# Kernel optimization log

Measured on AMD Instinct MI355X. Metric: run time of the kernel, lower is better.

## Reference

```python
import jax, jax.numpy as jnp
import numpy as np

B, D, K, L = 16384, 255, 4, 16  # batch, destinations, tunnels/dst, outgoing links
T = D * K                        # total tunnels = 1020
EPS = 1e-8


def setup_inputs() -> dict:
    key = jax.random.key(0)
    k1, k2, k3, k4, k5 = jax.random.split(key, 5)
    pred_ratios = jax.random.uniform(k1, (B, T), dtype=jnp.float32)
    demands = jax.random.uniform(k2, (B, D), dtype=jnp.float32) * 100.0
    current_link_utils = jax.random.uniform(k3, (B, L), dtype=jnp.float32)
    link_capacities = jax.random.uniform(k4, (L,), dtype=jnp.float32) * 900.0 + 100.0
    tunnel_to_link = jax.random.randint(k5, (T,), 0, L, dtype=jnp.int32)
    return {
        "pred_ratios": pred_ratios,
        "demands": demands,
        "current_link_utils": current_link_utils,
        "link_capacities": link_capacities,
        "tunnel_to_link": tunnel_to_link,
    }


def reference(pred_ratios, demands, current_link_utils, link_capacities, tunnel_to_link):
    # Equal group sizes: destination d owns tunnels [d*K, (d+1)*K)
    Tn = pred_ratios.shape[1]
    Dn = demands.shape[1]
    Kn = Tn // Dn
    Ln = link_capacities.shape[0]
    # tunnel_traffic[b, t] = demand[b, dst(t)] * ratio[b, t]
    tunnel_traffic = pred_ratios * jnp.repeat(demands, Kn, axis=1)  # [B, T]
    # scatter-add tunnels into links, expressed as a dense [T, L] one-hot GEMM
    onehot = jax.nn.one_hot(tunnel_to_link, Ln, dtype=pred_ratios.dtype)  # [T, L]
    node_link_traffic = tunnel_traffic @ onehot  # [B, L]
    node_link_util = node_link_traffic / (link_capacities[None, :] + EPS)
    variance_loss = jnp.var(node_link_util, axis=1, ddof=1).mean()  # torch.var is unbiased
    congestion_penalty = (node_link_util * current_link_utils).sum(axis=1).mean()
    max_util_loss = node_link_util.max(axis=1).mean()
    return 0.3 * variance_loss + 0.5 * congestion_penalty + 0.2 * max_util_loss
```

## Files before the change

kernel.cpp:

```cpp
#include <hip/hip_runtime.h>

constexpr int T_TUN = 1020;
constexpr int D_DST = 255;
constexpr int L_LNK = 16;
constexpr float EPS = 1e-8f;
constexpr int ROWS_PER_BLOCK = 8;
constexpr int ROWS_PER_WAVE  = 2;
constexpr int PSTRIDE = 16;

__global__ __launch_bounds__(256) void rowloss_kernel(
    const float* __restrict__ pred,
    const float* __restrict__ demands,
    const float* __restrict__ cur,
    const float* __restrict__ caps,
    const int*   __restrict__ t2l,
    float* __restrict__ partials)
{
  const int tid  = threadIdx.x;
  const int lane = tid & 63;
  const int w    = tid >> 6;

  __shared__ float priv_all[4][64 * PSTRIDE];
  __shared__ float wacc[4];
  float* priv = priv_all[w];
  float* mine = priv + lane * PSTRIDE;

  const int b16 = lane & 15;
  const float capinv = 1.0f / (caps[b16] + EPS);

  int off[4][4];
  bool dv[4];
#pragma unroll
  for (int j = 0; j < 4; ++j) {
    const int d = lane + 64 * j;
    dv[j] = (d < D_DST);
    const int dd = dv[j] ? d : 0;
    const int4 lk = ((const int4*)t2l)[dd];
    off[j][0] = lane * PSTRIDE + lk.x;
    off[j][1] = lane * PSTRIDE + lk.y;
    off[j][2] = lane * PSTRIDE + lk.z;
    off[j][3] = lane * PSTRIDE + lk.w;
  }

  float acc = 0.0f;
  const int row0 = blockIdx.x * ROWS_PER_BLOCK + w * ROWS_PER_WAVE;

#pragma unroll
  for (int r = 0; r < ROWS_PER_WAVE; ++r) {
    const int b = row0 + r;

    __builtin_amdgcn_wave_barrier();

    const float4 z = make_float4(0.f, 0.f, 0.f, 0.f);
    float4* mz = (float4*)mine;
    mz[0] = z; mz[1] = z; mz[2] = z; mz[3] = z;

    const float  mycur = cur[(size_t)b * L_LNK + b16];
    const float4* prow = (const float4*)(pred + (size_t)b * T_TUN);
    const float*  drow = demands + (size_t)b * D_DST;

#pragma unroll
    for (int j = 0; j < 4; ++j) {
      if (!dv[j]) continue;
      const int d = lane + 64 * j;
      const float4 r4 = prow[d];
      const float dem = drow[d];
      priv[off[j][0]] += r4.x * dem;
      priv[off[j][1]] += r4.y * dem;
      priv[off[j][2]] += r4.z * dem;
      priv[off[j][3]] += r4.w * dem;
    }

    __builtin_amdgcn_wave_barrier();

    float cs = 0.0f;
#pragma unroll
    for (int k = 0; k < 16; ++k) cs += priv[lane + 64 * k];
    cs += __shfl_xor(cs, 16, 64);
    cs += __shfl_xor(cs, 32, 64);

    const float u = cs * capinv;
    float s1 = u, s2 = u * u, s3 = u * mycur, mx = u;
#pragma unroll
    for (int m = 1; m < 16; m <<= 1) {
      s1 += __shfl_xor(s1, m, 64);
      s2 += __shfl_xor(s2, m, 64);
      s3 += __shfl_xor(s3, m, 64);
      const float o = __shfl_xor(mx, m, 64);
      mx = fmaxf(mx, o);
    }
    const float mean = s1 * (1.0f / 16.0f);
    const float var  = (s2 - 16.0f * mean * mean) * (1.0f / 15.0f);
    acc += 0.3f * var + 0.5f * s3 + 0.2f * mx;
  }

  if (lane == 0) wacc[w] = acc;
  __syncthreads();
  if (tid == 0) partials[blockIdx.x] = wacc[0] + wacc[1] + wacc[2] + wacc[3];
}

__global__ __launch_bounds__(256) void reduce_kernel(
    const float* __restrict__ partials, int n, float* __restrict__ out, float invB)
{
  __shared__ float s[256];
  const int tid = threadIdx.x;
  float a = 0.0f;
  for (int i = tid; i < n; i += 256) a += partials[i];
  s[tid] = a;
  __syncthreads();
  for (int st = 128; st > 0; st >>= 1) {
    if (tid < st) s[tid] += s[tid + st];
    __syncthreads();
  }
  if (tid == 0) out[0] = s[0] * invB;
}

extern "C" void kernel_launch(void* const* d_in, const int* in_sizes, int n_in,
                              void* d_out, int out_size, void* d_ws, size_t ws_size,
                              hipStream_t stream) {
  const float* pred    = (const float*)d_in[0];
  const float* demands = (const float*)d_in[1];
  const float* cur     = (const float*)d_in[2];
  const float* caps    = (const float*)d_in[3];
  const int*   t2l     = (const int*)d_in[4];
  float* out = (float*)d_out;

  const int L = in_sizes[3];
  const int B = in_sizes[2] / L;

  const int grid = B / ROWS_PER_BLOCK;
  float* partials = (float*)d_ws;

  rowloss_kernel<<<grid, 256, 0, stream>>>(pred, demands, cur, caps, t2l, partials);
  reduce_kernel<<<1, 256, 0, stream>>>(partials, grid, out, 1.0f / (float)B);
}
```

Baseline: 111.3 us.

## Transpose LDS histogram layout, use LDS atomics, merge reductions, drop reduce kernel

Reorganizes the per-wave shared histogram from lane-major with stride 16 to link-major with stride 64, and accumulates with LDS float atomics, which changes the bank-conflict pattern of the scatter. The column reads use a rotated index to avoid conflicts. The four butterfly reductions (sum, sum of squares, weighted sum, max) become one shuffle chain, with each 16-lane group handling one statistic, followed by readlanes. The final reduce kernel is replaced by a global atomicAdd per block plus a tiny zeroing kernel, which makes the summation order nondeterministic.

```diff
diff --git a/kernel.cpp b/kernel.cpp
--- a/kernel.cpp
+++ b/kernel.cpp
@@ -6,7 +6,11 @@
 constexpr float EPS = 1e-8f;
 constexpr int ROWS_PER_BLOCK = 8;
 constexpr int ROWS_PER_WAVE  = 2;
-constexpr int PSTRIDE = 16;
+
+__device__ __forceinline__ float read_lane_f(float v, int l) {
+  return __builtin_bit_cast(float,
+      __builtin_amdgcn_readlane(__builtin_bit_cast(int, v), l));
+}
 
 __global__ __launch_bounds__(256) void rowloss_kernel(
     const float* __restrict__ pred,
@@ -14,18 +18,18 @@
     const float* __restrict__ cur,
     const float* __restrict__ caps,
     const int*   __restrict__ t2l,
-    float* __restrict__ partials)
+    float* __restrict__ out, float invB)
 {
   const int tid  = threadIdx.x;
   const int lane = tid & 63;
   const int w    = tid >> 6;
 
-  __shared__ float priv_all[4][64 * PSTRIDE];
+  __shared__ float priv_all[4][L_LNK * 64];
   __shared__ float wacc[4];
   float* priv = priv_all[w];
-  float* mine = priv + lane * PSTRIDE;
 
   const int b16 = lane & 15;
+  const int g   = lane >> 4;
   const float capinv = 1.0f / (caps[b16] + EPS);
 
   int off[4][4];
@@ -36,11 +40,13 @@
     dv[j] = (d < D_DST);
     const int dd = dv[j] ? d : 0;
     const int4 lk = ((const int4*)t2l)[dd];
-    off[j][0] = lane * PSTRIDE + lk.x;
-    off[j][1] = lane * PSTRIDE + lk.y;
-    off[j][2] = lane * PSTRIDE + lk.z;
-    off[j][3] = lane * PSTRIDE + lk.w;
+    off[j][0] = lk.x * 64 + lane;
+    off[j][1] = lk.y * 64 + lane;
+    off[j][2] = lk.z * 64 + lane;
+    off[j][3] = lk.w * 64 + lane;
   }
+
+  const int rbase = b16 * 64 + g * 16;
 
   float acc = 0.0f;
   const int row0 = blockIdx.x * ROWS_PER_BLOCK + w * ROWS_PER_WAVE;
@@ -51,9 +57,12 @@
 
     __builtin_amdgcn_wave_barrier();
 
-    const float4 z = make_float4(0.f, 0.f, 0.f, 0.f);
-    float4* mz = (float4*)mine;
-    mz[0] = z; mz[1] = z; mz[2] = z; mz[3] = z;
+    {
+      const float4 z = make_float4(0.f, 0.f, 0.f, 0.f);
+      float4* pz = (float4*)priv;
+#pragma unroll
+      for (int i = 0; i < 4; ++i) pz[lane + 64 * i] = z;
+    }
 
     const float  mycur = cur[(size_t)b * L_LNK + b16];
     const float4* prow = (const float4*)(pred + (size_t)b * T_TUN);
@@ -65,55 +74,45 @@
       const int d = lane + 64 * j;
       const float4 r4 = prow[d];
       const float dem = drow[d];
-      priv[off[j][0]] += r4.x * dem;
-      priv[off[j][1]] += r4.y * dem;
-      priv[off[j][2]] += r4.z * dem;
-      priv[off[j][3]] += r4.w * dem;
+      unsafeAtomicAdd(&priv[off[j][0]], r4.x * dem);
+      unsafeAtomicAdd(&priv[off[j][1]], r4.y * dem);
+      unsafeAtomicAdd(&priv[off[j][2]], r4.z * dem);
+      unsafeAtomicAdd(&priv[off[j][3]], r4.w * dem);
     }
 
     __builtin_amdgcn_wave_barrier();
 
     float cs = 0.0f;
 #pragma unroll
-    for (int k = 0; k < 16; ++k) cs += priv[lane + 64 * k];
+    for (int k = 0; k < 16; ++k) cs += priv[rbase + ((k + b16) & 15)];
     cs += __shfl_xor(cs, 16, 64);
     cs += __shfl_xor(cs, 32, 64);
 
     const float u = cs * capinv;
-    float s1 = u, s2 = u * u, s3 = u * mycur, mx = u;
+
+    float val = (g == 0) ? u : (g == 1) ? (u * u) : (g == 2) ? (u * mycur) : u;
 #pragma unroll
     for (int m = 1; m < 16; m <<= 1) {
-      s1 += __shfl_xor(s1, m, 64);
-      s2 += __shfl_xor(s2, m, 64);
-      s3 += __shfl_xor(s3, m, 64);
-      const float o = __shfl_xor(mx, m, 64);
-      mx = fmaxf(mx, o);
+      const float o  = __shfl_xor(val, m, 64);
+      const float sm = val + o;
+      const float mm = fmaxf(val, o);
+      val = (g == 3) ? mm : sm;
     }
-    const float mean = s1 * (1.0f / 16.0f);
-    const float var  = (s2 - 16.0f * mean * mean) * (1.0f / 15.0f);
+    const float s1 = read_lane_f(val, 0);
+    const float s2 = read_lane_f(val, 16);
+    const float s3 = read_lane_f(val, 32);
+    const float mx = read_lane_f(val, 48);
+
+    const float var = (s2 - s1 * s1 * (1.0f / 16.0f)) * (1.0f / 15.0f);
     acc += 0.3f * var + 0.5f * s3 + 0.2f * mx;
   }
 
   if (lane == 0) wacc[w] = acc;
   __syncthreads();
-  if (tid == 0) partials[blockIdx.x] = wacc[0] + wacc[1] + wacc[2] + wacc[3];
+  if (tid == 0) atomicAdd(out, (wacc[0] + wacc[1] + wacc[2] + wacc[3]) * invB);
 }
 
-__global__ __launch_bounds__(256) void reduce_kernel(
-    const float* __restrict__ partials, int n, float* __restrict__ out, float invB)
-{
-  __shared__ float s[256];
-  const int tid = threadIdx.x;
-  float a = 0.0f;
-  for (int i = tid; i < n; i += 256) a += partials[i];
-  s[tid] = a;
-  __syncthreads();
-  for (int st = 128; st > 0; st >>= 1) {
-    if (tid < st) s[tid] += s[tid + st];
-    __syncthreads();
-  }
-  if (tid == 0) out[0] = s[0] * invB;
-}
+__global__ void zero_out_kernel(float* __restrict__ out) { out[0] = 0.0f; }
 
 extern "C" void kernel_launch(void* const* d_in, const int* in_sizes, int n_in,
                               void* d_out, int out_size, void* d_ws, size_t ws_size,
@@ -129,8 +128,8 @@
   const int B = in_sizes[2] / L;
 
   const int grid = B / ROWS_PER_BLOCK;
-  float* partials = (float*)d_ws;
 
-  rowloss_kernel<<<grid, 256, 0, stream>>>(pred, demands, cur, caps, t2l, partials);
-  reduce_kernel<<<1, 256, 0, stream>>>(partials, grid, out, 1.0f / (float)B);
+  zero_out_kernel<<<1, 1, 0, stream>>>(out);
+  rowloss_kernel<<<grid, 256, 0, stream>>>(pred, demands, cur, caps, t2l,
+                                           out, 1.0f / (float)B);
 }
```

Result: slower. 180.4 us (+62.0%).
